# Kernel optimization log

Hardware: AMD Instinct MI355X
Metric: run time of the kernel (lower is better)

The kernel has to match this reference:

```python
import jax, jax.numpy as jnp
import numpy as np

EPS = 1e-5
K_GROUP = 8  # k_group_size


def setup_inputs() -> dict:
    key = jax.random.key(0)
    ks = jax.random.split(key, 8)
    C = 384  # encoder_channel
    rn = lambda k, s: (jax.random.normal(k, s, dtype=jnp.float32) * 0.05)
    return {
        "point_groups": jax.random.normal(ks[0], (4, 256, 32, 3), dtype=jnp.float32),
        # first_conv: Conv1d(3,128,1)+BN+ReLU+Conv1d(128,256,1)
        "W1": rn(ks[1], (128, 3)), "b1": jnp.zeros(128, jnp.float32),
        "gamma1": jnp.ones(128, jnp.float32), "beta1": jnp.zeros(128, jnp.float32),
        "W2": rn(ks[2], (256, 128)), "b2": jnp.zeros(256, jnp.float32),
        # second_conv: Conv1d(512,512,1)+BN+ReLU+Conv1d(512,C,1)
        "W3": rn(ks[3], (512, 512)), "b3": jnp.zeros(512, jnp.float32),
        "gamma3": jnp.ones(512, jnp.float32), "beta3": jnp.zeros(512, jnp.float32),
        "W4": rn(ks[4], (C, 512)), "b4": jnp.zeros(C, jnp.float32),
        # K_Norm affine (out_dim = C, matching declared parameter shapes)
        "alpha": jnp.ones((1, 1, 1, C), jnp.float32),
        "beta_aff": jnp.zeros((1, 1, 1, C), jnp.float32),
        # fusion_layer: Conv1d(2C,C,1)+BN+ReLU
        "Wf": rn(ks[5], (C, 2 * C)), "bf": jnp.zeros(C, jnp.float32),
        "gammaf": jnp.ones(C, jnp.float32), "betaf": jnp.zeros(C, jnp.float32),
    }


def _conv1x1(x, W, b):  # x: (B,Cin,L), W: (Cout,Cin)
    return jnp.einsum("bcl,oc->bol", x, W) + b[None, :, None]


def _bn(x, gamma, beta):  # training-mode BatchNorm1d over (batch, length)
    mu = jnp.mean(x, axis=(0, 2), keepdims=True)
    var = jnp.var(x, axis=(0, 2), keepdims=True)
    xh = (x - mu) * jax.lax.rsqrt(var + EPS)
    return xh * gamma[None, :, None] + beta[None, :, None]


def reference(point_groups, W1, b1, gamma1, beta1, W2, b2, W3, b3, gamma3, beta3,
              W4, b4, alpha, beta_aff, Wf, bf, gammaf, betaf):
    bs, g, n, _ = point_groups.shape
    C = W4.shape[0]
    pg = point_groups.reshape(bs * g, n, 3)  # (B', n, 3)

    # first_conv stack
    f = _conv1x1(pg.transpose(0, 2, 1), W1, b1)           # (B',128,n)
    f = jax.nn.relu(_bn(f, gamma1, beta1))
    f = _conv1x1(f, W2, b2)                               # (B',256,n)
    fg = jnp.max(f, axis=2, keepdims=True)                # (B',256,1)
    f = jnp.concatenate([jnp.broadcast_to(fg, f.shape), f], axis=1)  # (B',512,n)

    # second_conv stack
    f = _conv1x1(f, W3, b3)
    f = jax.nn.relu(_bn(f, gamma3, beta3))
    f = _conv1x1(f, W4, b4)                               # (B',C,n)
    feat = f.transpose(0, 2, 1)                           # (B',n,C)

    # KNN within each group (self included, as in KNN(xyz,xyz))
    sq = jnp.sum(pg * pg, axis=-1)                        # (B',n)
    d = sq[:, :, None] + sq[:, None, :] - 2.0 * jnp.einsum("bnc,bmc->bnm", pg, pg)
    _, idx = jax.lax.top_k(-d, K_GROUP)                   # (B',n,K)

    gather = jax.vmap(lambda a, i: a[i])
    knn_x = gather(feat, idx)                             # (B',n,K,C)

    # K_Norm: center-relative normalization by global scalar std (torch.std, ddof=1)
    mean_x = feat[:, :, None, :]
    dx = knn_x - mean_x
    std_x = jnp.std(dx, ddof=1)
    knn_x = dx / (std_x + EPS)
    knn_x = alpha * knn_x + beta_aff                      # (B',n,K,C)

    enhanced = jnp.mean(knn_x, axis=2)                    # mean over K -> (B',n,C)
    enhanced = jnp.mean(enhanced, axis=1)                 # pool over n -> (B',C)

    fg2 = jnp.max(f, axis=2)                              # (B',C)
    fused_in = jnp.concatenate([fg2, enhanced], axis=1)[:, :, None]  # (B',2C,1)
    fused = jax.nn.relu(_bn(_conv1x1(fused_in, Wf, bf), gammaf, betaf))[:, :, 0]
    return fused.reshape(bs, g, C)
```

## Files before the change

kernel.cpp:

```cpp
#include <hip/hip_runtime.h>
#include <math.h>

#define EPS 1e-5f

typedef __attribute__((ext_vector_type(8))) short s16x8;
typedef __attribute__((ext_vector_type(4))) float f32x4;

__device__ __forceinline__ unsigned short f2bf(float x) {
    unsigned u = __float_as_uint(x);
    u += 0x7fffu + ((u >> 16) & 1u);
    return (unsigned short)(u >> 16);
}
__device__ __forceinline__ float bf2f(unsigned short h) {
    return __uint_as_float(((unsigned)h) << 16);
}
__device__ __forceinline__ unsigned long long pack4bf(float a, float b, float c, float d) {
    return (unsigned long long)f2bf(a)
         | ((unsigned long long)f2bf(b) << 16)
         | ((unsigned long long)f2bf(c) << 32)
         | ((unsigned long long)f2bf(d) << 48);
}

__global__ __launch_bounds__(128) void k1_conv1_knn(
    const float* __restrict__ pg, const float* __restrict__ W1,
    const float* __restrict__ b1,
    const float* __restrict__ W2, const float* __restrict__ W3,
    const float* __restrict__ W4, const float* __restrict__ Wf,
    unsigned short* __restrict__ h1b, float* __restrict__ p1s, float* __restrict__ p1q,
    int* __restrict__ idxw,
    unsigned short* __restrict__ W2b, unsigned short* __restrict__ W3b,
    unsigned short* __restrict__ W4b, unsigned short* __restrict__ Wfb)
{
    __shared__ float pgs[96];
    __shared__ float sqs[32];
    if (blockIdx.x >= 1024) {
        const int i = (blockIdx.x - 1024) * 128 + threadIdx.x;
        if (i < 32768)  W2b[i] = f2bf(W2[i]);
        if (i < 262144) W3b[i] = f2bf(W3[i]);
        if (i < 196608) W4b[i] = f2bf(W4[i]);
        if (i < 294912) Wfb[i] = f2bf(Wf[i]);
        return;
    }
    const int b = blockIdx.x;
    const int t = threadIdx.x;
    if (t < 96) pgs[t] = pg[b * 96 + t];
    __syncthreads();
    if (t < 32) {
        float x = pgs[t*3+0], y = pgs[t*3+1], z = pgs[t*3+2];
        sqs[t] = x*x + y*y + z*z;
    }
    __syncthreads();
    {
        const float w0 = W1[t*3+0], w1 = W1[t*3+1], w2 = W1[t*3+2];
        const float bb = b1[t];
        float s = 0.f, q = 0.f;
        unsigned short* hcol = h1b + (size_t)b*4096 + t;
        #pragma unroll
        for (int l = 0; l < 32; ++l) {
            float v = fmaf(w2, pgs[l*3+2], fmaf(w1, pgs[l*3+1], fmaf(w0, pgs[l*3+0], bb)));
            hcol[l*128] = f2bf(v); s += v; q += v*v;
        }
        p1s[b*128 + t] = s;
        p1q[b*128 + t] = q;
    }
    if (t < 32) {
        const float xl = pgs[t*3+0], yl = pgs[t*3+1], zl = pgs[t*3+2];
        const float sql = sqs[t];
        float dist[32];
        #pragma unroll
        for (int m = 0; m < 32; ++m) {
            float dot = xl*pgs[m*3+0] + yl*pgs[m*3+1] + zl*pgs[m*3+2];
            dist[m] = sql + sqs[m] - 2.f*dot;
        }
        unsigned used = 0u;
        int* orow = idxw + b*256 + t*8;
        #pragma unroll
        for (int j = 0; j < 8; ++j) {
            float best = 3.4e38f; int bi = 0;
            #pragma unroll
            for (int m = 0; m < 32; ++m) {
                if (!((used >> m) & 1u) && dist[m] < best) { best = dist[m]; bi = m; }
            }
            used |= (1u << bi);
            orow[j] = bi;
        }
    }
}

__global__ __launch_bounds__(256) void k_bn_fin2(
    const float* __restrict__ ps, const float* __restrict__ pq,
    int nPart, int nChan, float invN,
    const float* __restrict__ gamma, const float* __restrict__ beta,
    float* __restrict__ scale, float* __restrict__ shift)
{
    const int ob = blockIdx.x * 4;
    const int t = threadIdx.x;
    const int co = t & 3, i0 = t >> 2;
    float s = 0.f, q = 0.f;
    for (int i = i0; i < nPart; i += 64) {
        s += ps[(size_t)i*nChan + ob + co];
        q += pq[(size_t)i*nChan + ob + co];
    }
    #pragma unroll
    for (int off = 32; off >= 4; off >>= 1) {
        s += __shfl_down(s, off, 64);
        q += __shfl_down(q, off, 64);
    }
    __shared__ float ss[4][4], qs[4][4];
    const int wid = t >> 6, lane = t & 63;
    if (lane < 4) { ss[wid][lane] = s; qs[wid][lane] = q; }
    __syncthreads();
    if (t < 4) {
        float S = ss[0][t] + ss[1][t] + ss[2][t] + ss[3][t];
        float Q = qs[0][t] + qs[1][t] + qs[2][t] + qs[3][t];
        const int o = ob + t;
        float mu  = S * invN;
        float var = Q * invN - mu*mu;
        float sc  = gamma[o] * rsqrtf(var + EPS);
        scale[o] = sc;
        shift[o] = beta[o] - mu * sc;
    }
}

__global__ __launch_bounds__(512, 2) void k3_mfma(
    const unsigned short* __restrict__ h1b,
    const float* __restrict__ scale1, const float* __restrict__ shift1,
    const unsigned short* __restrict__ W2b, const float* __restrict__ b2,
    const unsigned short* __restrict__ W3b, const float* __restrict__ b3,
    unsigned short* __restrict__ h3b, float* __restrict__ p3s, float* __restrict__ p3q)
{
    const int g0 = blockIdx.x * 2;
    const int t = threadIdx.x;
    __shared__ __align__(16) unsigned short SB[19472];
    unsigned short* B1  = SB;
    unsigned short* F2  = SB;
    unsigned short* FGB = SB + 16896;
    float* FGR = (float*)(SB + 17424);

    {
        const int l = t >> 3, c0 = (t & 7) * 16;
        const int g = g0 + (l >> 5);
        #pragma unroll
        for (int h = 0; h < 2; ++h) {
            s16x8 hv = *(const s16x8*)(h1b + (size_t)g*4096 + (l & 31)*128 + c0 + h*8);
            unsigned short ov[8];
            #pragma unroll
            for (int e = 0; e < 8; ++e) {
                int c = c0 + h*8 + e;
                float v = fmaxf(fmaf(bf2f((unsigned short)hv[e]), scale1[c], shift1[c]), 0.f);
                ov[e] = f2bf(v);
            }
            uint4 o4;
            o4.x = (unsigned)ov[0] | ((unsigned)ov[1] << 16);
            o4.y = (unsigned)ov[2] | ((unsigned)ov[3] << 16);
            o4.z = (unsigned)ov[4] | ((unsigned)ov[5] << 16);
            o4.w = (unsigned)ov[6] | ((unsigned)ov[7] << 16);
            *(uint4*)&B1[l*136 + c0 + h*8] = o4;
        }
    }
    __syncthreads();

    const int wave = t >> 6;
    const int lane = t & 63;
    const int m    = lane & 15;
    const int quad = lane >> 4;

    f32x4 acc2[2][4];
    #pragma unroll
    for (int mt = 0; mt < 2; ++mt)
        #pragma unroll
        for (int n = 0; n < 4; ++n)
            acc2[mt][n] = (f32x4){0.f, 0.f, 0.f, 0.f};

    #pragma unroll
    for (int kt = 0; kt < 4; ++kt) {
        s16x8 bv[4];
        #pragma unroll
        for (int nt = 0; nt < 4; ++nt)
            bv[nt] = *(const s16x8*)&B1[(nt*16 + m)*136 + kt*32 + quad*8];
        #pragma unroll
        for (int mt = 0; mt < 2; ++mt) {
            s16x8 av = *(const s16x8*)(W2b + (size_t)(wave*32 + mt*16 + m)*128 + kt*32 + quad*8);
            #pragma unroll
            for (int nt = 0; nt < 4; ++nt)
                acc2[mt][nt] = __builtin_amdgcn_mfma_f32_16x16x32_bf16(av, bv[nt], acc2[mt][nt], 0, 0, 0);
        }
    }
    __syncthreads();

    #pragma unroll
    for (int mt = 0; mt < 2; ++mt) {
        const int o0 = wave*32 + mt*16 + quad*4;
        #pragma unroll
        for (int r = 0; r < 4; ++r) {
            float bb = b2[o0 + r];
            #pragma unroll
            for (int nt = 0; nt < 4; ++nt) acc2[mt][nt][r] += bb;
        }
        #pragma unroll
        for (int nt = 0; nt < 4; ++nt) {
            const int row = nt*16 + m;
            *(unsigned long long*)&F2[row*264 + o0] =
                pack4bf(acc2[mt][nt][0], acc2[mt][nt][1], acc2[mt][nt][2], acc2[mt][nt][3]);
        }
        float f0[4], f1[4];
        #pragma unroll
        for (int r = 0; r < 4; ++r) {
            f0[r] = fmaxf(acc2[mt][0][r], acc2[mt][1][r]);
            f1[r] = fmaxf(acc2[mt][2][r], acc2[mt][3][r]);
        }
        #pragma unroll
        for (int msk = 1; msk < 16; msk <<= 1)
            #pragma unroll
            for (int r = 0; r < 4; ++r) {
                f0[r] = fmaxf(f0[r], __shfl_xor(f0[r], msk, 16));
                f1[r] = fmaxf(f1[r], __shfl_xor(f1[r], msk, 16));
            }
        if (m == 0) {
            *(unsigned long long*)&FGB[o0]       = pack4bf(f0[0], f0[1], f0[2], f0[3]);
            *(unsigned long long*)&FGB[264 + o0] = pack4bf(f1[0], f1[1], f1[2], f1[3]);
        }
    }
    __syncthreads();

    {
        f32x4 facc[4];
        #pragma unroll
        for (int i = 0; i < 4; ++i) facc[i] = (f32x4){0.f, 0.f, 0.f, 0.f};
        #pragma unroll
        for (int kt = 0; kt < 8; ++kt) {
            s16x8 bg = *(const s16x8*)&FGB[(m & 1)*264 + kt*32 + quad*8];
            #pragma unroll
            for (int i = 0; i < 4; ++i) {
                s16x8 av = *(const s16x8*)(W3b + (size_t)((wave*4 + i)*16 + m)*512 + kt*32 + quad*8);
                facc[i] = __builtin_amdgcn_mfma_f32_16x16x32_bf16(av, bg, facc[i], 0, 0, 0);
            }
        }
        if (m < 2) {
            #pragma unroll
            for (int i = 0; i < 4; ++i)
                #pragma unroll
                for (int r = 0; r < 4; ++r)
                    FGR[((wave*4 + i)*16 + quad*4 + r)*2 + m] = facc[i][r];
        }
    }
    __syncthreads();

    f32x4 acc3[4][4];
    #pragma unroll
    for (int mt = 0; mt < 4; ++mt) {
        const int ob = (wave*4 + mt)*16 + quad*4;
        #pragma unroll
        for (int r = 0; r < 4; ++r) {
            float2 fb = *(const float2*)&FGR[(ob + r)*2];
            float bb = b3[ob + r];
            acc3[mt][0][r] = bb + fb.x;
            acc3[mt][1][r] = bb + fb.x;
            acc3[mt][2][r] = bb + fb.y;
            acc3[mt][3][r] = bb + fb.y;
        }
    }
    #pragma unroll 4
    for (int kt = 0; kt < 8; ++kt) {
        s16x8 bv[4];
        #pragma unroll
        for (int nt = 0; nt < 4; ++nt)
            bv[nt] = *(const s16x8*)&F2[(nt*16 + m)*264 + kt*32 + quad*8];
        #pragma unroll
        for (int mt = 0; mt < 4; ++mt) {
            s16x8 av = *(const s16x8*)(W3b + (size_t)((wave*4 + mt)*16 + m)*512 + 256 + kt*32 + quad*8);
            #pragma unroll
            for (int nt = 0; nt < 4; ++nt)
                acc3[mt][nt] = __builtin_amdgcn_mfma_f32_16x16x32_bf16(av, bv[nt], acc3[mt][nt], 0, 0, 0);
        }
    }

    unsigned short* dst = h3b + (size_t)blockIdx.x * 32768;
    #pragma unroll
    for (int mt = 0; mt < 4; ++mt) {
        const int ot = wave*4 + mt;
        const int o0 = ot*16 + quad*4;
        float s0[4], q0[4], s1[4], q1[4];
        #pragma unroll
        for (int r = 0; r < 4; ++r) {
            s0[r] = acc3[mt][0][r] + acc3[mt][1][r];
            q0[r] = acc3[mt][0][r]*acc3[mt][0][r] + acc3[mt][1][r]*acc3[mt][1][r];
            s1[r] = acc3[mt][2][r] + acc3[mt][3][r];
            q1[r] = acc3[mt][2][r]*acc3[mt][2][r] + acc3[mt][3][r]*acc3[mt][3][r];
        }
        {
            unsigned long long u0 = pack4bf(acc3[mt][0][0], acc3[mt][0][1], acc3[mt][0][2], acc3[mt][0][3]);
            unsigned long long u1 = pack4bf(acc3[mt][1][0], acc3[mt][1][1], acc3[mt][1][2], acc3[mt][1][3]);
            unsigned long long u2 = pack4bf(acc3[mt][2][0], acc3[mt][2][1], acc3[mt][2][2], acc3[mt][2][3]);
            unsigned long long u3 = pack4bf(acc3[mt][3][0], acc3[mt][3][1], acc3[mt][3][2], acc3[mt][3][3]);
            unsigned short* p = dst + (size_t)(ot*64 + lane) * 16;
            *(uint4*)(p)     = make_uint4((unsigned)u0, (unsigned)(u0 >> 32), (unsigned)u1, (unsigned)(u1 >> 32));
            *(uint4*)(p + 8) = make_uint4((unsigned)u2, (unsigned)(u2 >> 32), (unsigned)u3, (unsigned)(u3 >> 32));
        }
        #pragma unroll
        for (int msk = 1; msk < 16; msk <<= 1)
            #pragma unroll
            for (int r = 0; r < 4; ++r) {
                s0[r] += __shfl_xor(s0[r], msk, 16);
                q0[r] += __shfl_xor(q0[r], msk, 16);
                s1[r] += __shfl_xor(s1[r], msk, 16);
                q1[r] += __shfl_xor(q1[r], msk, 16);
            }
        if (m == 0) {
            #pragma unroll
            for (int r = 0; r < 4; ++r) {
                p3s[(size_t)g0*512 + o0 + r]       = s0[r];
                p3q[(size_t)g0*512 + o0 + r]       = q0[r];
                p3s[(size_t)(g0+1)*512 + o0 + r]   = s1[r];
                p3q[(size_t)(g0+1)*512 + o0 + r]   = q1[r];
            }
        }
    }
}

__global__ __launch_bounds__(768, 2) void k5_mfma(
    const unsigned short* __restrict__ h3b,
    const float* __restrict__ scale3, const float* __restrict__ shift3,
    const unsigned short* __restrict__ W4b, const float* __restrict__ b4,
    const int* __restrict__ idxw,
    float* __restrict__ fg2, float* __restrict__ A,
    float* __restrict__ S1p, float* __restrict__ S2p)
{
    const int g0 = blockIdx.x * 2;
    const int t = threadIdx.x;
    __shared__ __align__(16) unsigned short SB[33280];
    unsigned short* B4 = SB;
    unsigned short* XT = SB;
    unsigned short* Mm = SB + 30720;
    __shared__ int icnt[2][32];
    __shared__ float r1[2][12], r2[2][12];

    {
        const uint4* src = (const uint4*)(h3b + (size_t)blockIdx.x * 32768);
        for (int i = t; i < 4096; i += 768) {
            uint4 hv = src[i];
            const int flat16 = i >> 1, half = i & 1;
            const int ln = flat16 & 63, m2 = ln & 15, q2 = ln >> 4;
            const int wm = flat16 >> 6;
            const int o0 = wm*16 + q2*4;
            const float4 sc = *(const float4*)(scale3 + o0);
            const float4 sh = *(const float4*)(shift3 + o0);
            const int rowa = (half*2)*16 + m2;
            float a0 = fmaxf(fmaf(bf2f((unsigned short)(hv.x       )), sc.x, sh.x), 0.f);
            float a1 = fmaxf(fmaf(bf2f((unsigned short)(hv.x >> 16 )), sc.y, sh.y), 0.f);
            float a2 = fmaxf(fmaf(bf2f((unsigned short)(hv.y       )), sc.z, sh.z), 0.f);
            float a3 = fmaxf(fmaf(bf2f((unsigned short)(hv.y >> 16 )), sc.w, sh.w), 0.f);
            float b0 = fmaxf(fmaf(bf2f((unsigned short)(hv.z       )), sc.x, sh.x), 0.f);
            float b1 = fmaxf(fmaf(bf2f((unsigned short)(hv.z >> 16 )), sc.y, sh.y), 0.f);
            float b2 = fmaxf(fmaf(bf2f((unsigned short)(hv.w       )), sc.z, sh.z), 0.f);
            float b3 = fmaxf(fmaf(bf2f((unsigned short)(hv.w >> 16 )), sc.w, sh.w), 0.f);
            *(unsigned long long*)&B4[rowa*520 + o0]        = pack4bf(a0, a1, a2, a3);
            *(unsigned long long*)&B4[(rowa + 16)*520 + o0] = pack4bf(b0, b1, b2, b3);
        }
    }
    if (t < 64) icnt[t >> 5][t & 31] = 0;
    __syncthreads();

    const int wave = t >> 6;
    const int lane = t & 63;
    const int m    = lane & 15;
    const int quad = lane >> 4;

    f32x4 acc4[2][4];
    #pragma unroll
    for (int mt = 0; mt < 2; ++mt)
        #pragma unroll
        for (int n = 0; n < 4; ++n)
            acc4[mt][n] = (f32x4){0.f, 0.f, 0.f, 0.f};

    #pragma unroll 4
    for (int kt = 0; kt < 16; ++kt) {
        s16x8 bv[4];
        #pragma unroll
        for (int nt = 0; nt < 4; ++nt)
            bv[nt] = *(const s16x8*)&B4[(nt*16 + m)*520 + kt*32 + quad*8];
        #pragma unroll
        for (int mt = 0; mt < 2; ++mt) {
            s16x8 av = *(const s16x8*)(W4b + (size_t)(wave*32 + mt*16 + m)*512 + kt*32 + quad*8);
            #pragma unroll
            for (int nt = 0; nt < 4; ++nt)
                acc4[mt][nt] = __builtin_amdgcn_mfma_f32_16x16x32_bf16(av, bv[nt], acc4[mt][nt], 0, 0, 0);
        }
    }

    #pragma unroll
    for (int mt = 0; mt < 2; ++mt) {
        const int o0 = wave*32 + mt*16 + quad*4;
        float f0[4], f1[4];
        #pragma unroll
        for (int r = 0; r < 4; ++r) {
            float bb = b4[o0 + r];
            #pragma unroll
            for (int nt = 0; nt < 4; ++nt) acc4[mt][nt][r] += bb;
            f0[r] = fmaxf(acc4[mt][0][r], acc4[mt][1][r]);
            f1[r] = fmaxf(acc4[mt][2][r], acc4[mt][3][r]);
        }
        #pragma unroll
        for (int msk = 1; msk < 16; msk <<= 1)
            #pragma unroll
            for (int r = 0; r < 4; ++r) {
                f0[r] = fmaxf(f0[r], __shfl_xor(f0[r], msk, 16));
                f1[r] = fmaxf(f1[r], __shfl_xor(f1[r], msk, 16));
            }
        if (m == 0) {
            #pragma unroll
            for (int r = 0; r < 4; ++r) {
                fg2[(size_t)g0*384 + o0 + r]     = f0[r];
                fg2[(size_t)(g0+1)*384 + o0 + r] = f1[r];
            }
        }
    }
    __syncthreads();

    #pragma unroll
    for (int mt = 0; mt < 2; ++mt) {
        const int o0 = wave*32 + mt*16 + quad*4;
        #pragma unroll
        for (int nt = 0; nt < 4; ++nt) {
            const int g = nt >> 1;
            const int l = (nt & 1)*16 + m;
            unsigned short* xg = XT + g*15360;
            #pragma unroll
            for (int r = 0; r < 4; ++r)
                xg[(o0 + r)*40 + l] = f2bf(acc4[mt][nt][r]);
        }
    }
    if (t < 64) {
        const int g = t >> 5, l = t & 31;
        uint4 z = make_uint4(0u, 0u, 0u, 0u);
        #pragma unroll
        for (int i = 0; i < 5; ++i)
            *(uint4*)&Mm[g*1280 + l*40 + i*8] = z;
    }
    __syncthreads();

    if (t < 64) {
        const int g = t >> 5, l = t & 31;
        const int* ip = idxw + (size_t)(g0 + g)*256 + l*8;
        #pragma unroll
        for (int j = 0; j < 8; ++j) {
            int ix = ip[j];
            Mm[g*1280 + l*40 + ix] = 0x3F80;
            atomicAdd(&icnt[g][ix], 1);
        }
    }
    __syncthreads();

    float s1loc[2] = {0.f, 0.f}, s2loc[2] = {0.f, 0.f};
    #pragma unroll
    for (int g = 0; g < 2; ++g) {
        const float c0 = (float)icnt[g][m];
        const float c1 = (float)icnt[g][m + 16];
        const float w0 = c0 - 8.f, u0 = c0 + 8.f;
        const float w1 = c1 - 8.f, u1 = c1 + 8.f;
        #pragma unroll
        for (int mt = 0; mt < 2; ++mt) {
            const int o0 = wave*32 + mt*16 + quad*4;
            float Ap[4];
            #pragma unroll
            for (int r = 0; r < 4; ++r) {
                const float x0 = acc4[mt][g*2 + 0][r];
                const float x1 = acc4[mt][g*2 + 1][r];
                Ap[r] = w0*x0 + w1*x1;
                s1loc[g] += Ap[r];
                s2loc[g] += u0*x0*x0 + u1*x1*x1;
            }
            #pragma unroll
            for (int msk = 1; msk < 16; msk <<= 1)
                #pragma unroll
                for (int r = 0; r < 4; ++r)
                    Ap[r] += __shfl_xor(Ap[r], msk, 16);
            if (m == 0) {
                #pragma unroll
                for (int r = 0; r < 4; ++r)
                    A[(size_t)(g0 + g)*384 + o0 + r] = Ap[r];
            }
        }
    }

    #pragma unroll
    for (int g = 0; g < 2; ++g) {
        const unsigned short* xg = XT + g*15360;
        float cross = 0.f;
        #pragma unroll
        for (int lt = 0; lt < 2; ++lt) {
            s16x8 af = *(const s16x8*)&Mm[g*1280 + (lt*16 + m)*40 + quad*8];
            #pragma unroll
            for (int i = 0; i < 2; ++i) {
                const int oc = (wave*2 + i)*16 + m;
                s16x8 bfv = *(const s16x8*)&xg[oc*40 + quad*8];
                f32x4 sa = __builtin_amdgcn_mfma_f32_16x16x32_bf16(
                    af, bfv, (f32x4){0.f, 0.f, 0.f, 0.f}, 0, 0, 0);
                #pragma unroll
                for (int r = 0; r < 4; ++r) {
                    const int lp = lt*16 + quad*4 + r;
                    cross = fmaf(bf2f(xg[oc*40 + lp]), sa[r], cross);
                }
            }
        }
        s2loc[g] -= 2.f * cross;
    }

    #pragma unroll
    for (int g = 0; g < 2; ++g) {
        float sA = s1loc[g], sQ = s2loc[g];
        #pragma unroll
        for (int off = 32; off > 0; off >>= 1) {
            sA += __shfl_down(sA, off, 64);
            sQ += __shfl_down(sQ, off, 64);
        }
        if (lane == 0) { r1[g][wave] = sA; r2[g][wave] = sQ; }
    }
    __syncthreads();
    if (t < 2) {
        float S = 0.f, Q = 0.f;
        #pragma unroll
        for (int w = 0; w < 12; ++w) { S += r1[t][w]; Q += r2[t][w]; }
        S1p[g0 + t] = S;
        S2p[g0 + t] = Q;
    }
}

__global__ __launch_bounds__(384) void k7_fused(
    const float* __restrict__ fg2, const float* __restrict__ A,
    const float* __restrict__ alpha, const float* __restrict__ beta_aff,
    const float* __restrict__ S1p, const float* __restrict__ S2p,
    const unsigned short* __restrict__ Wfb, const float* __restrict__ bf,
    float* __restrict__ hf, float* __restrict__ pfs, float* __restrict__ pfq)
{
    const int blk = blockIdx.x;
    const int g0 = blk * 16;
    const int t = threadIdx.x;
    __shared__ __align__(16) char smem[24832];
    unsigned short* xfb = (unsigned short*)smem;
    float* OTf = (float*)smem;
    __shared__ double rs[6], rq[6];
    __shared__ float stdsh;

    {
        double s = 0.0, q = 0.0;
        for (int i = t; i < 1024; i += 384) { s += (double)S1p[i]; q += (double)S2p[i]; }
        #pragma unroll
        for (int off = 32; off > 0; off >>= 1) {
            s += __shfl_down(s, off, 64);
            q += __shfl_down(q, off, 64);
        }
        if ((t & 63) == 0) { rs[t >> 6] = s; rq[t >> 6] = q; }
        __syncthreads();
        if (t == 0) {
            double S = 0.0, Q = 0.0;
            #pragma unroll
            for (int w = 0; w < 6; ++w) { S += rs[w]; Q += rq[w]; }
            const double N = 1024.0 * 32.0 * 8.0 * 384.0;
            double var = (Q - S*S/N) / (N - 1.0);
            stdsh = (float)sqrt(var);
        }
        __syncthreads();
    }
    const float inv = 1.f / (256.f * (stdsh + EPS));

    for (int i = t; i < 16*96; i += 384) {
        const int row = i / 96, c8 = (i % 96) * 8;
        const int g = g0 + row;
        float e[8];
        if (c8 < 384) {
            const float4* s0 = (const float4*)(fg2 + (size_t)g*384 + c8);
            float4 v0 = s0[0], v1 = s0[1];
            e[0]=v0.x; e[1]=v0.y; e[2]=v0.z; e[3]=v0.w;
            e[4]=v1.x; e[5]=v1.y; e[6]=v1.z; e[7]=v1.w;
        } else {
            const int cc = c8 - 384;
            const float4* s0 = (const float4*)(A + (size_t)g*384 + cc);
            float4 v0 = s0[0], v1 = s0[1];
            float av[8] = {v0.x,v0.y,v0.z,v0.w,v1.x,v1.y,v1.z,v1.w};
            #pragma unroll
            for (int j = 0; j < 8; ++j)
                e[j] = fmaf(alpha[cc+j] * inv, av[j], beta_aff[cc+j]);
        }
        uint4 o4;
        o4.x = (unsigned)f2bf(e[0]) | ((unsigned)f2bf(e[1]) << 16);
        o4.y = (unsigned)f2bf(e[2]) | ((unsigned)f2bf(e[3]) << 16);
        o4.z = (unsigned)f2bf(e[4]) | ((unsigned)f2bf(e[5]) << 16);
        o4.w = (unsigned)f2bf(e[6]) | ((unsigned)f2bf(e[7]) << 16);
        *(uint4*)&xfb[row*776 + c8] = o4;
    }
    __syncthreads();

    const int wave = t >> 6;
    const int lane = t & 63;
    const int m    = lane & 15;
    const int quad = lane >> 4;

    f32x4 acc[4];
    #pragma unroll
    for (int mt = 0; mt < 4; ++mt) acc[mt] = (f32x4){0.f, 0.f, 0.f, 0.f};

    #pragma unroll 4
    for (int kt = 0; kt < 24; ++kt) {
        s16x8 bv = *(const s16x8*)&xfb[m*776 + kt*32 + quad*8];
        #pragma unroll
        for (int mt = 0; mt < 4; ++mt) {
            s16x8 av = *(const s16x8*)(Wfb + (size_t)(wave*64 + mt*16 + m)*768 + kt*32 + quad*8);
            acc[mt] = __builtin_amdgcn_mfma_f32_16x16x32_bf16(av, bv, acc[mt], 0, 0, 0);
        }
    }

    #pragma unroll
    for (int mt = 0; mt < 4; ++mt) {
        const int o0 = wave*64 + mt*16 + quad*4;
        float s[4], q[4];
        #pragma unroll
        for (int r = 0; r < 4; ++r) {
            acc[mt][r] += bf[o0 + r];
            s[r] = acc[mt][r];
            q[r] = acc[mt][r]*acc[mt][r];
        }
        #pragma unroll
        for (int msk = 1; msk < 16; msk <<= 1)
            #pragma unroll
            for (int r = 0; r < 4; ++r) {
                s[r] += __shfl_xor(s[r], msk, 16);
                q[r] += __shfl_xor(q[r], msk, 16);
            }
        if (m == 0) {
            #pragma unroll
            for (int r = 0; r < 4; ++r) {
                pfs[(size_t)blk*384 + o0 + r] = s[r];
                pfq[(size_t)blk*384 + o0 + r] = q[r];
            }
        }
    }
    __syncthreads();

    #pragma unroll
    for (int mt = 0; mt < 4; ++mt) {
        const int o0 = wave*64 + mt*16 + quad*4;
        #pragma unroll
        for (int r = 0; r < 4; ++r)
            OTf[m*388 + o0 + r] = acc[mt][r];
    }
    __syncthreads();

    {
        float* dst = hf + (size_t)g0*384;
        #pragma unroll
        for (int k = 0; k < 4; ++k) {
            const int i = t + k*384;
            const int row = i / 96;
            float4 v = *(const float4*)&OTf[i*4 + row*4];
            *(float4*)(dst + i*4) = v;
        }
    }
}

__global__ __launch_bounds__(384) void k9_out(
    const float* __restrict__ hf,
    const float* __restrict__ pfs, const float* __restrict__ pfq,
    const float* __restrict__ gammaf, const float* __restrict__ betaf,
    float* __restrict__ out)
{
    const int blk = blockIdx.x, t = threadIdx.x;
    float S = 0.f, Q = 0.f;
    #pragma unroll 8
    for (int i = 0; i < 64; ++i) {
        S += pfs[(size_t)i*384 + t];
        Q += pfq[(size_t)i*384 + t];
    }
    const float mu  = S * (1.f/1024.f);
    const float var = Q * (1.f/1024.f) - mu*mu;
    const float sc  = gammaf[t] * rsqrtf(var + EPS);
    const float sh  = betaf[t] - mu * sc;
    const size_t base = (size_t)blk * 8 * 384;
    #pragma unroll
    for (int g = 0; g < 8; ++g) {
        float v = fmaf(hf[base + g*384 + t], sc, sh);
        out[base + g*384 + t] = fmaxf(v, 0.f);
    }
}

extern "C" void kernel_launch(void* const* d_in, const int* in_sizes, int n_in,
                              void* d_out, int out_size, void* d_ws, size_t ws_size,
                              hipStream_t stream) {
    const float* pg      = (const float*)d_in[0];
    const float* W1      = (const float*)d_in[1];
    const float* b1      = (const float*)d_in[2];
    const float* gamma1  = (const float*)d_in[3];
    const float* beta1   = (const float*)d_in[4];
    const float* W2      = (const float*)d_in[5];
    const float* b2      = (const float*)d_in[6];
    const float* W3      = (const float*)d_in[7];
    const float* b3      = (const float*)d_in[8];
    const float* gamma3  = (const float*)d_in[9];
    const float* beta3   = (const float*)d_in[10];
    const float* W4      = (const float*)d_in[11];
    const float* b4      = (const float*)d_in[12];
    const float* alpha   = (const float*)d_in[13];
    const float* beta_af = (const float*)d_in[14];
    const float* Wf      = (const float*)d_in[15];
    const float* bf      = (const float*)d_in[16];
    const float* gammaf  = (const float*)d_in[17];
    const float* betaf   = (const float*)d_in[18];
    float* out = (float*)d_out;

    float* w = (float*)d_ws;
    unsigned short* h1b = (unsigned short*)w; w += 1024*4096/2;
    unsigned short* h3b = (unsigned short*)w; w += 1024*16384/2;
    unsigned short* W2b = (unsigned short*)w; w += 32768/2;
    unsigned short* W3b = (unsigned short*)w; w += 262144/2;
    unsigned short* W4b = (unsigned short*)w; w += 196608/2;
    unsigned short* Wfb = (unsigned short*)w; w += 294912/2;
    float* hf     = w;  w += 1024*384;
    float* fg2    = w;  w += 1024*384;
    float* A      = w;  w += 1024*384;
    float* p1s    = w;  w += 1024*128;
    float* p1q    = w;  w += 1024*128;
    float* p3s    = w;  w += 1024*512;
    float* p3q    = w;  w += 1024*512;
    float* pfs    = w;  w += 64*384;
    float* pfq    = w;  w += 64*384;
    float* S1p    = w;  w += 1024;
    float* S2p    = w;  w += 1024;
    float* scale1 = w;  w += 128;
    float* shift1 = w;  w += 128;
    float* scale3 = w;  w += 512;
    float* shift3 = w;  w += 512;
    int*   idxw   = (int*)w;  w += 1024*256;

    hipLaunchKernelGGL(k1_conv1_knn, dim3(1024 + 2304), dim3(128), 0, stream,
                       pg, W1, b1, W2, W3, W4, Wf,
                       h1b, p1s, p1q, idxw, W2b, W3b, W4b, Wfb);
    hipLaunchKernelGGL(k_bn_fin2, dim3(32), dim3(256), 0, stream,
                       p1s, p1q, 1024, 128, 1.f/32768.f, gamma1, beta1, scale1, shift1);
    hipLaunchKernelGGL(k3_mfma, dim3(512), dim3(512), 0, stream,
                       h1b, scale1, shift1, W2b, b2, W3b, b3, h3b, p3s, p3q);
    hipLaunchKernelGGL(k_bn_fin2, dim3(128), dim3(256), 0, stream,
                       p3s, p3q, 1024, 512, 1.f/32768.f, gamma3, beta3, scale3, shift3);
    hipLaunchKernelGGL(k5_mfma, dim3(512), dim3(768), 0, stream,
                       h3b, scale3, shift3, W4b, b4, idxw, fg2, A, S1p, S2p);
    hipLaunchKernelGGL(k7_fused, dim3(64), dim3(384), 0, stream,
                       fg2, A, alpha, beta_af, S1p, S2p, Wfb, bf, hf, pfs, pfq);
    hipLaunchKernelGGL(k9_out, dim3(128), dim3(384), 0, stream,
                       hf, pfs, pfq, gammaf, betaf, out);
}
```

Measured before the change: 236.2 us.

## Process one group per block in k3 and k5, doubling grid size

k3_mfma and k5_mfma now handle a single point group per block instead of two. Shared memory and accumulators are halved, and k5 uses 384 threads with 4 M-tiles per wave. The grids double to 1024 blocks and the launch bounds allow more resident blocks, aiming for better occupancy and latency hiding. In exchange, each weight tile loaded from W2/W3/W4 is reused across only 32 columns instead of 64, which raises weight traffic per unit of work.

```diff
diff --git a/kernel.cpp b/kernel.cpp
--- a/kernel.cpp
+++ b/kernel.cpp
@@ -122,41 +122,37 @@
     }
 }
 
-__global__ __launch_bounds__(512, 2) void k3_mfma(
+__global__ __launch_bounds__(512, 4) void k3_mfma(
     const unsigned short* __restrict__ h1b,
     const float* __restrict__ scale1, const float* __restrict__ shift1,
     const unsigned short* __restrict__ W2b, const float* __restrict__ b2,
     const unsigned short* __restrict__ W3b, const float* __restrict__ b3,
     unsigned short* __restrict__ h3b, float* __restrict__ p3s, float* __restrict__ p3q)
 {
-    const int g0 = blockIdx.x * 2;
+    const int g = blockIdx.x;
     const int t = threadIdx.x;
-    __shared__ __align__(16) unsigned short SB[19472];
+    __shared__ __align__(16) unsigned short SB[9736];
     unsigned short* B1  = SB;
     unsigned short* F2  = SB;
-    unsigned short* FGB = SB + 16896;
-    float* FGR = (float*)(SB + 17424);
-
-    {
-        const int l = t >> 3, c0 = (t & 7) * 16;
-        const int g = g0 + (l >> 5);
-        #pragma unroll
-        for (int h = 0; h < 2; ++h) {
-            s16x8 hv = *(const s16x8*)(h1b + (size_t)g*4096 + (l & 31)*128 + c0 + h*8);
-            unsigned short ov[8];
-            #pragma unroll
-            for (int e = 0; e < 8; ++e) {
-                int c = c0 + h*8 + e;
-                float v = fmaxf(fmaf(bf2f((unsigned short)hv[e]), scale1[c], shift1[c]), 0.f);
-                ov[e] = f2bf(v);
-            }
-            uint4 o4;
-            o4.x = (unsigned)ov[0] | ((unsigned)ov[1] << 16);
-            o4.y = (unsigned)ov[2] | ((unsigned)ov[3] << 16);
-            o4.z = (unsigned)ov[4] | ((unsigned)ov[5] << 16);
-            o4.w = (unsigned)ov[6] | ((unsigned)ov[7] << 16);
-            *(uint4*)&B1[l*136 + c0 + h*8] = o4;
-        }
+    unsigned short* FGB = SB + 8448;
+    float* FGR = (float*)(SB + 8712);
+
+    {
+        const int l = t >> 4, c0 = (t & 15) * 8;
+        s16x8 hv = *(const s16x8*)(h1b + (size_t)g*4096 + l*128 + c0);
+        unsigned short ov[8];
+        #pragma unroll
+        for (int e = 0; e < 8; ++e) {
+            int c = c0 + e;
+            float v = fmaxf(fmaf(bf2f((unsigned short)hv[e]), scale1[c], shift1[c]), 0.f);
+            ov[e] = f2bf(v);
+        }
+        uint4 o4;
+        o4.x = (unsigned)ov[0] | ((unsigned)ov[1] << 16);
+        o4.y = (unsigned)ov[2] | ((unsigned)ov[3] << 16);
+        o4.z = (unsigned)ov[4] | ((unsigned)ov[5] << 16);
+        o4.w = (unsigned)ov[6] | ((unsigned)ov[7] << 16);
+        *(uint4*)&B1[l*136 + c0] = o4;
     }
     __syncthreads();
 
@@ -165,24 +161,24 @@
     const int m    = lane & 15;
     const int quad = lane >> 4;
 
-    f32x4 acc2[2][4];
+    f32x4 acc2[2][2];
     #pragma unroll
     for (int mt = 0; mt < 2; ++mt)
         #pragma unroll
-        for (int n = 0; n < 4; ++n)
+        for (int n = 0; n < 2; ++n)
             acc2[mt][n] = (f32x4){0.f, 0.f, 0.f, 0.f};
 
     #pragma unroll
     for (int kt = 0; kt < 4; ++kt) {
-        s16x8 bv[4];
-        #pragma unroll
-        for (int nt = 0; nt < 4; ++nt)
+        s16x8 bv[2];
+        #pragma unroll
+        for (int nt = 0; nt < 2; ++nt)
             bv[nt] = *(const s16x8*)&B1[(nt*16 + m)*136 + kt*32 + quad*8];
         #pragma unroll
         for (int mt = 0; mt < 2; ++mt) {
             s16x8 av = *(const s16x8*)(W2b + (size_t)(wave*32 + mt*16 + m)*128 + kt*32 + quad*8);
             #pragma unroll
-            for (int nt = 0; nt < 4; ++nt)
+            for (int nt = 0; nt < 2; ++nt)
                 acc2[mt][nt] = __builtin_amdgcn_mfma_f32_16x16x32_bf16(av, bv[nt], acc2[mt][nt], 0, 0, 0);
         }
     }
@@ -195,31 +191,25 @@
         for (int r = 0; r < 4; ++r) {
             float bb = b2[o0 + r];
             #pragma unroll
-            for (int nt = 0; nt < 4; ++nt) acc2[mt][nt][r] += bb;
-        }
-        #pragma unroll
-        for (int nt = 0; nt < 4; ++nt) {
+            for (int nt = 0; nt < 2; ++nt) acc2[mt][nt][r] += bb;
+        }
+        #pragma unroll
+        for (int nt = 0; nt < 2; ++nt) {
             const int row = nt*16 + m;
             *(unsigned long long*)&F2[row*264 + o0] =
                 pack4bf(acc2[mt][nt][0], acc2[mt][nt][1], acc2[mt][nt][2], acc2[mt][nt][3]);
         }
-        float f0[4], f1[4];
-        #pragma unroll
-        for (int r = 0; r < 4; ++r) {
+        float f0[4];
+        #pragma unroll
+        for (int r = 0; r < 4; ++r)
             f0[r] = fmaxf(acc2[mt][0][r], acc2[mt][1][r]);
-            f1[r] = fmaxf(acc2[mt][2][r], acc2[mt][3][r]);
-        }
         #pragma unroll
         for (int msk = 1; msk < 16; msk <<= 1)
             #pragma unroll
-            for (int r = 0; r < 4; ++r) {
+            for (int r = 0; r < 4; ++r)
                 f0[r] = fmaxf(f0[r], __shfl_xor(f0[r], msk, 16));
-                f1[r] = fmaxf(f1[r], __shfl_xor(f1[r], msk, 16));
-            }
-        if (m == 0) {
-            *(unsigned long long*)&FGB[o0]       = pack4bf(f0[0], f0[1], f0[2], f0[3]);
-            *(unsigned long long*)&FGB[264 + o0] = pack4bf(f1[0], f1[1], f1[2], f1[3]);
-        }
+        if (m == 0)
+            *(unsigned long long*)&FGB[o0] = pack4bf(f0[0], f0[1], f0[2], f0[3]);
     }
     __syncthreads();
 
@@ -229,73 +219,65 @@
         for (int i = 0; i < 4; ++i) facc[i] = (f32x4){0.f, 0.f, 0.f, 0.f};
         #pragma unroll
         for (int kt = 0; kt < 8; ++kt) {
-            s16x8 bg = *(const s16x8*)&FGB[(m & 1)*264 + kt*32 + quad*8];
+            s16x8 bg = *(const s16x8*)&FGB[kt*32 + quad*8];
             #pragma unroll
             for (int i = 0; i < 4; ++i) {
                 s16x8 av = *(const s16x8*)(W3b + (size_t)((wave*4 + i)*16 + m)*512 + kt*32 + quad*8);
                 facc[i] = __builtin_amdgcn_mfma_f32_16x16x32_bf16(av, bg, facc[i], 0, 0, 0);
             }
         }
-        if (m < 2) {
+        if (m == 0) {
             #pragma unroll
             for (int i = 0; i < 4; ++i)
                 #pragma unroll
                 for (int r = 0; r < 4; ++r)
-                    FGR[((wave*4 + i)*16 + quad*4 + r)*2 + m] = facc[i][r];
-        }
-    }
-    __syncthreads();
-
-    f32x4 acc3[4][4];
+                    FGR[(wave*4 + i)*16 + quad*4 + r] = facc[i][r];
+        }
+    }
+    __syncthreads();
+
+    f32x4 acc3[4][2];
     #pragma unroll
     for (int mt = 0; mt < 4; ++mt) {
         const int ob = (wave*4 + mt)*16 + quad*4;
         #pragma unroll
         for (int r = 0; r < 4; ++r) {
-            float2 fb = *(const float2*)&FGR[(ob + r)*2];
-            float bb = b3[ob + r];
-            acc3[mt][0][r] = bb + fb.x;
-            acc3[mt][1][r] = bb + fb.x;
-            acc3[mt][2][r] = bb + fb.y;
-            acc3[mt][3][r] = bb + fb.y;
+            float base = b3[ob + r] + FGR[ob + r];
+            acc3[mt][0][r] = base;
+            acc3[mt][1][r] = base;
         }
     }
     #pragma unroll 4
     for (int kt = 0; kt < 8; ++kt) {
-        s16x8 bv[4];
-        #pragma unroll
-        for (int nt = 0; nt < 4; ++nt)
+        s16x8 bv[2];
+        #pragma unroll
+        for (int nt = 0; nt < 2; ++nt)
             bv[nt] = *(const s16x8*)&F2[(nt*16 + m)*264 + kt*32 + quad*8];
         #pragma unroll
         for (int mt = 0; mt < 4; ++mt) {
             s16x8 av = *(const s16x8*)(W3b + (size_t)((wave*4 + mt)*16 + m)*512 + 256 + kt*32 + quad*8);
             #pragma unroll
-            for (int nt = 0; nt < 4; ++nt)
+            for (int nt = 0; nt < 2; ++nt)
                 acc3[mt][nt] = __builtin_amdgcn_mfma_f32_16x16x32_bf16(av, bv[nt], acc3[mt][nt], 0, 0, 0);
         }
     }
 
-    unsigned short* dst = h3b + (size_t)blockIdx.x * 32768;
+    unsigned short* dst = h3b + (size_t)g * 16384;
     #pragma unroll
     for (int mt = 0; mt < 4; ++mt) {
         const int ot = wave*4 + mt;
         const int o0 = ot*16 + quad*4;
-        float s0[4], q0[4], s1[4], q1[4];
+        float s0[4], q0[4];
         #pragma unroll
         for (int r = 0; r < 4; ++r) {
             s0[r] = acc3[mt][0][r] + acc3[mt][1][r];
             q0[r] = acc3[mt][0][r]*acc3[mt][0][r] + acc3[mt][1][r]*acc3[mt][1][r];
-            s1[r] = acc3[mt][2][r] + acc3[mt][3][r];
-            q1[r] = acc3[mt][2][r]*acc3[mt][2][r] + acc3[mt][3][r]*acc3[mt][3][r];
         }
         {
             unsigned long long u0 = pack4bf(acc3[mt][0][0], acc3[mt][0][1], acc3[mt][0][2], acc3[mt][0][3]);
             unsigned long long u1 = pack4bf(acc3[mt][1][0], acc3[mt][1][1], acc3[mt][1][2], acc3[mt][1][3]);
-            unsigned long long u2 = pack4bf(acc3[mt][2][0], acc3[mt][2][1], acc3[mt][2][2], acc3[mt][2][3]);
-            unsigned long long u3 = pack4bf(acc3[mt][3][0], acc3[mt][3][1], acc3[mt][3][2], acc3[mt][3][3]);
-            unsigned short* p = dst + (size_t)(ot*64 + lane) * 16;
-            *(uint4*)(p)     = make_uint4((unsigned)u0, (unsigned)(u0 >> 32), (unsigned)u1, (unsigned)(u1 >> 32));
-            *(uint4*)(p + 8) = make_uint4((unsigned)u2, (unsigned)(u2 >> 32), (unsigned)u3, (unsigned)(u3 >> 32));
+            unsigned short* p = dst + (size_t)(ot*64 + lane) * 8;
+            *(uint4*)(p) = make_uint4((unsigned)u0, (unsigned)(u0 >> 32), (unsigned)u1, (unsigned)(u1 >> 32));
         }
         #pragma unroll
         for (int msk = 1; msk < 16; msk <<= 1)
@@ -303,22 +285,18 @@
             for (int r = 0; r < 4; ++r) {
                 s0[r] += __shfl_xor(s0[r], msk, 16);
                 q0[r] += __shfl_xor(q0[r], msk, 16);
-                s1[r] += __shfl_xor(s1[r], msk, 16);
-                q1[r] += __shfl_xor(q1[r], msk, 16);
             }
         if (m == 0) {
             #pragma unroll
             for (int r = 0; r < 4; ++r) {
-                p3s[(size_t)g0*512 + o0 + r]       = s0[r];
-                p3q[(size_t)g0*512 + o0 + r]       = q0[r];
-                p3s[(size_t)(g0+1)*512 + o0 + r]   = s1[r];
-                p3q[(size_t)(g0+1)*512 + o0 + r]   = q1[r];
-            }
-        }
-    }
-}
-
-__global__ __launch_bounds__(768, 2) void k5_mfma(
+                p3s[(size_t)g*512 + o0 + r] = s0[r];
+                p3q[(size_t)g*512 + o0 + r] = q0[r];
+            }
+        }
+    }
+}
+
+__global__ __launch_bounds__(384, 4) void k5_mfma(
     const unsigned short* __restrict__ h3b,
     const float* __restrict__ scale3, const float* __restrict__ shift3,
     const unsigned short* __restrict__ W4b, const float* __restrict__ b4,
@@ -326,26 +304,24 @@
     float* __restrict__ fg2, float* __restrict__ A,
     float* __restrict__ S1p, float* __restrict__ S2p)
 {
-    const int g0 = blockIdx.x * 2;
+    const int g = blockIdx.x;
     const int t = threadIdx.x;
-    __shared__ __align__(16) unsigned short SB[33280];
+    __shared__ __align__(16) unsigned short SB[16640];
     unsigned short* B4 = SB;
     unsigned short* XT = SB;
-    unsigned short* Mm = SB + 30720;
-    __shared__ int icnt[2][32];
-    __shared__ float r1[2][12], r2[2][12];
-
-    {
-        const uint4* src = (const uint4*)(h3b + (size_t)blockIdx.x * 32768);
-        for (int i = t; i < 4096; i += 768) {
+    unsigned short* Mm = SB + 15360;
+    __shared__ int icnt[32];
+    __shared__ float r1[6], r2[6];
+
+    {
+        const uint4* src = (const uint4*)(h3b + (size_t)g * 16384);
+        for (int i = t; i < 2048; i += 384) {
             uint4 hv = src[i];
-            const int flat16 = i >> 1, half = i & 1;
-            const int ln = flat16 & 63, m2 = ln & 15, q2 = ln >> 4;
-            const int wm = flat16 >> 6;
-            const int o0 = wm*16 + q2*4;
+            const int ln = i & 63, m2 = ln & 15, q2 = ln >> 4;
+            const int ot = i >> 6;
+            const int o0 = ot*16 + q2*4;
             const float4 sc = *(const float4*)(scale3 + o0);
             const float4 sh = *(const float4*)(shift3 + o0);
-            const int rowa = (half*2)*16 + m2;
             float a0 = fmaxf(fmaf(bf2f((unsigned short)(hv.x       )), sc.x, sh.x), 0.f);
             float a1 = fmaxf(fmaf(bf2f((unsigned short)(hv.x >> 16 )), sc.y, sh.y), 0.f);
             float a2 = fmaxf(fmaf(bf2f((unsigned short)(hv.y       )), sc.z, sh.z), 0.f);
@@ -354,11 +330,10 @@
             float b1 = fmaxf(fmaf(bf2f((unsigned short)(hv.z >> 16 )), sc.y, sh.y), 0.f);
             float b2 = fmaxf(fmaf(bf2f((unsigned short)(hv.w       )), sc.z, sh.z), 0.f);
             float b3 = fmaxf(fmaf(bf2f((unsigned short)(hv.w >> 16 )), sc.w, sh.w), 0.f);
-            *(unsigned long long*)&B4[rowa*520 + o0]        = pack4bf(a0, a1, a2, a3);
-            *(unsigned long long*)&B4[(rowa + 16)*520 + o0] = pack4bf(b0, b1, b2, b3);
-        }
-    }
-    if (t < 64) icnt[t >> 5][t & 31] = 0;
+            *(unsigned long long*)&B4[m2*520 + o0]        = pack4bf(a0, a1, a2, a3);
+            *(unsigned long long*)&B4[(m2 + 16)*520 + o0] = pack4bf(b0, b1, b2, b3);
+        }
+    }
     __syncthreads();
 
     const int wave = t >> 6;
@@ -366,109 +341,100 @@
     const int m    = lane & 15;
     const int quad = lane >> 4;
 
-    f32x4 acc4[2][4];
-    #pragma unroll
-    for (int mt = 0; mt < 2; ++mt)
-        #pragma unroll
-        for (int n = 0; n < 4; ++n)
+    f32x4 acc4[4][2];
+    #pragma unroll
+    for (int mt = 0; mt < 4; ++mt)
+        #pragma unroll
+        for (int n = 0; n < 2; ++n)
             acc4[mt][n] = (f32x4){0.f, 0.f, 0.f, 0.f};
 
     #pragma unroll 4
     for (int kt = 0; kt < 16; ++kt) {
-        s16x8 bv[4];
-        #pragma unroll
-        for (int nt = 0; nt < 4; ++nt)
+        s16x8 bv[2];
+        #pragma unroll
+        for (int nt = 0; nt < 2; ++nt)
             bv[nt] = *(const s16x8*)&B4[(nt*16 + m)*520 + kt*32 + quad*8];
         #pragma unroll
-        for (int mt = 0; mt < 2; ++mt) {
-            s16x8 av = *(const s16x8*)(W4b + (size_t)(wave*32 + mt*16 + m)*512 + kt*32 + quad*8);
-            #pragma unroll
-            for (int nt = 0; nt < 4; ++nt)
+        for (int mt = 0; mt < 4; ++mt) {
+            s16x8 av = *(const s16x8*)(W4b + (size_t)((wave*4 + mt)*16 + m)*512 + kt*32 + quad*8);
+            #pragma unroll
+            for (int nt = 0; nt < 2; ++nt)
                 acc4[mt][nt] = __builtin_amdgcn_mfma_f32_16x16x32_bf16(av, bv[nt], acc4[mt][nt], 0, 0, 0);
         }
     }
 
     #pragma unroll
-    for (int mt = 0; mt < 2; ++mt) {
-        const int o0 = wave*32 + mt*16 + quad*4;
-        float f0[4], f1[4];
+    for (int mt = 0; mt < 4; ++mt) {
+        const int o0 = (wave*4 + mt)*16 + quad*4;
+        float f0[4];
         #pragma unroll
         for (int r = 0; r < 4; ++r) {
             float bb = b4[o0 + r];
-            #pragma unroll
-            for (int nt = 0; nt < 4; ++nt) acc4[mt][nt][r] += bb;
+            acc4[mt][0][r] += bb;
+            acc4[mt][1][r] += bb;
             f0[r] = fmaxf(acc4[mt][0][r], acc4[mt][1][r]);
-            f1[r] = fmaxf(acc4[mt][2][r], acc4[mt][3][r]);
         }
         #pragma unroll
         for (int msk = 1; msk < 16; msk <<= 1)
             #pragma unroll
-            for (int r = 0; r < 4; ++r) {
+            for (int r = 0; r < 4; ++r)
                 f0[r] = fmaxf(f0[r], __shfl_xor(f0[r], msk, 16));
-                f1[r] = fmaxf(f1[r], __shfl_xor(f1[r], msk, 16));
-            }
         if (m == 0) {
             #pragma unroll
-            for (int r = 0; r < 4; ++r) {
-                fg2[(size_t)g0*384 + o0 + r]     = f0[r];
-                fg2[(size_t)(g0+1)*384 + o0 + r] = f1[r];
-            }
-        }
-    }
-    __syncthreads();
-
-    #pragma unroll
-    for (int mt = 0; mt < 2; ++mt) {
-        const int o0 = wave*32 + mt*16 + quad*4;
-        #pragma unroll
-        for (int nt = 0; nt < 4; ++nt) {
-            const int g = nt >> 1;
-            const int l = (nt & 1)*16 + m;
-            unsigned short* xg = XT + g*15360;
-            #pragma unroll
             for (int r = 0; r < 4; ++r)
-                xg[(o0 + r)*40 + l] = f2bf(acc4[mt][nt][r]);
-        }
-    }
-    if (t < 64) {
-        const int g = t >> 5, l = t & 31;
+                fg2[(size_t)g*384 + o0 + r] = f0[r];
+        }
+    }
+    __syncthreads();
+
+    #pragma unroll
+    for (int mt = 0; mt < 4; ++mt) {
+        const int o0 = (wave*4 + mt)*16 + quad*4;
+        #pragma unroll
+        for (int nt = 0; nt < 2; ++nt) {
+            const int l = nt*16 + m;
+            #pragma unroll
+            for (int r = 0; r < 4; ++r)
+                XT[(o0 + r)*40 + l] = f2bf(acc4[mt][nt][r]);
+        }
+    }
+    if (t < 32) {
         uint4 z = make_uint4(0u, 0u, 0u, 0u);
         #pragma unroll
         for (int i = 0; i < 5; ++i)
-            *(uint4*)&Mm[g*1280 + l*40 + i*8] = z;
-    }
-    __syncthreads();
-
-    if (t < 64) {
-        const int g = t >> 5, l = t & 31;
-        const int* ip = idxw + (size_t)(g0 + g)*256 + l*8;
+            *(uint4*)&Mm[t*40 + i*8] = z;
+        icnt[t] = 0;
+    }
+    __syncthreads();
+
+    if (t < 32) {
+        const int* ip = idxw + (size_t)g*256 + t*8;
         #pragma unroll
         for (int j = 0; j < 8; ++j) {
             int ix = ip[j];
-            Mm[g*1280 + l*40 + ix] = 0x3F80;
-            atomicAdd(&icnt[g][ix], 1);
-        }
-    }
-    __syncthreads();
-
-    float s1loc[2] = {0.f, 0.f}, s2loc[2] = {0.f, 0.f};
-    #pragma unroll
-    for (int g = 0; g < 2; ++g) {
-        const float c0 = (float)icnt[g][m];
-        const float c1 = (float)icnt[g][m + 16];
+            Mm[t*40 + ix] = 0x3F80;
+            atomicAdd(&icnt[ix], 1);
+        }
+    }
+    __syncthreads();
+
+    float s1loc = 0.f, s2loc = 0.f;
+    {
+        const float c0 = (float)icnt[m];
+        const float c1 = (float)icnt[m + 16];
         const float w0 = c0 - 8.f, u0 = c0 + 8.f;
         const float w1 = c1 - 8.f, u1 = c1 + 8.f;
         #pragma unroll
-        for (int mt = 0; mt < 2; ++mt) {
-            const int o0 = wave*32 + mt*16 + quad*4;
+        for (int mt = 0; mt < 4; ++mt) {
+            const int o0 = (wave*4 + mt)*16 + quad*4;
             float Ap[4];
             #pragma unroll
             for (int r = 0; r < 4; ++r) {
-                const float x0 = acc4[mt][g*2 + 0][r];
-                const float x1 = acc4[mt][g*2 + 1][r];
+                const float x0 = acc4[mt][0][r];
+                const float x1 = acc4[mt][1][r];
                 Ap[r] = w0*x0 + w1*x1;
-                s1loc[g] += Ap[r];
-                s2loc[g] += u0*x0*x0 + u1*x1*x1;
+                s1loc += Ap[r];
+                s2loc += u0*x0*x0 + u1*x1*x1;
             }
             #pragma unroll
             for (int msk = 1; msk < 16; msk <<= 1)
@@ -478,51 +444,45 @@
             if (m == 0) {
                 #pragma unroll
                 for (int r = 0; r < 4; ++r)
-                    A[(size_t)(g0 + g)*384 + o0 + r] = Ap[r];
-            }
-        }
-    }
-
-    #pragma unroll
-    for (int g = 0; g < 2; ++g) {
-        const unsigned short* xg = XT + g*15360;
+                    A[(size_t)g*384 + o0 + r] = Ap[r];
+            }
+        }
+    }
+
+    {
         float cross = 0.f;
         #pragma unroll
         for (int lt = 0; lt < 2; ++lt) {
-            s16x8 af = *(const s16x8*)&Mm[g*1280 + (lt*16 + m)*40 + quad*8];
-            #pragma unroll
-            for (int i = 0; i < 2; ++i) {
-                const int oc = (wave*2 + i)*16 + m;
-                s16x8 bfv = *(const s16x8*)&xg[oc*40 + quad*8];
+            s16x8 af = *(const s16x8*)&Mm[(lt*16 + m)*40 + quad*8];
+            #pragma unroll
+            for (int i = 0; i < 4; ++i) {
+                const int oc = (wave*4 + i)*16 + m;
+                s16x8 bfv = *(const s16x8*)&XT[oc*40 + quad*8];
                 f32x4 sa = __builtin_amdgcn_mfma_f32_16x16x32_bf16(
                     af, bfv, (f32x4){0.f, 0.f, 0.f, 0.f}, 0, 0, 0);
                 #pragma unroll
                 for (int r = 0; r < 4; ++r) {
                     const int lp = lt*16 + quad*4 + r;
-                    cross = fmaf(bf2f(xg[oc*40 + lp]), sa[r], cross);
+                    cross = fmaf(bf2f(XT[oc*40 + lp]), sa[r], cross);
                 }
             }
         }
-        s2loc[g] -= 2.f * cross;
-    }
-
-    #pragma unroll
-    for (int g = 0; g < 2; ++g) {
-        float sA = s1loc[g], sQ = s2loc[g];
+        s2loc -= 2.f * cross;
+    }
+
+    {
+        float sA = s1loc, sQ = s2loc;
         #pragma unroll
         for (int off = 32; off > 0; off >>= 1) {
             sA += __shfl_down(sA, off, 64);
             sQ += __shfl_down(sQ, off, 64);
         }
-        if (lane == 0) { r1[g][wave] = sA; r2[g][wave] = sQ; }
-    }
-    __syncthreads();
-    if (t < 2) {
-        float S = 0.f, Q = 0.f;
-        #pragma unroll
-        for (int w = 0; w < 12; ++w) { S += r1[t][w]; Q += r2[t][w]; }
-        S1p[g0 + t] = S;
-        S2p[g0 + t] = Q;
+        if (lane == 0) { r1[wave] = sA; r2[wave] = sQ; }
+    }
+    __syncthreads();
+    if (t == 0) {
+        S1p[g] = r1[0]+r1[1]+r1[2]+r1[3]+r1[4]+r1[5];
+        S2p[g] = r2[0]+r2[1]+r2[2]+r2[3]+r2[4]+r2[5];
     }
 }
 
@@ -736,11 +696,11 @@
                        h1b, p1s, p1q, idxw, W2b, W3b, W4b, Wfb);
     hipLaunchKernelGGL(k_bn_fin2, dim3(32), dim3(256), 0, stream,
                        p1s, p1q, 1024, 128, 1.f/32768.f, gamma1, beta1, scale1, shift1);
-    hipLaunchKernelGGL(k3_mfma, dim3(512), dim3(512), 0, stream,
+    hipLaunchKernelGGL(k3_mfma, dim3(1024), dim3(512), 0, stream,
                        h1b, scale1, shift1, W2b, b2, W3b, b3, h3b, p3s, p3q);
     hipLaunchKernelGGL(k_bn_fin2, dim3(128), dim3(256), 0, stream,
                        p3s, p3q, 1024, 512, 1.f/32768.f, gamma3, beta3, scale3, shift3);
-    hipLaunchKernelGGL(k5_mfma, dim3(512), dim3(768), 0, stream,
+    hipLaunchKernelGGL(k5_mfma, dim3(1024), dim3(384), 0, stream,
                        h3b, scale3, shift3, W4b, b4, idxw, fg2, A, S1p, S2p);
     hipLaunchKernelGGL(k7_fused, dim3(64), dim3(384), 0, stream,
                        fg2, A, alpha, beta_af, S1p, S2p, Wfb, bf, hf, pfs, pfq);
```

New measurement: 283.6 us. 20.1% more time.
